# Kernel tuning notes

Measured on AMD Instinct MI355X. Metric: run time of the kernel, lower is better.

The kernel has to match this reference:

```python
import jax, jax.numpy as jnp
import numpy as np

N_NODES = 50000
N_EDGES = 800000
IN_FEAT = 128
HIDDEN = 128
NUM_CLASS = 40


def setup_inputs() -> dict:
    key = jax.random.key(0)
    ks = jax.random.split(key, 8)
    feat = jax.random.normal(ks[0], (N_NODES, IN_FEAT), dtype=jnp.float32)
    # Glorot-ish init scale for reference weights
    W1 = jax.random.normal(ks[1], (IN_FEAT, HIDDEN), dtype=jnp.float32) / np.sqrt(IN_FEAT)
    b1 = jnp.zeros((HIDDEN,), dtype=jnp.float32)
    W2 = jax.random.normal(ks[2], (HIDDEN, HIDDEN), dtype=jnp.float32) / np.sqrt(HIDDEN)
    b2 = jnp.zeros((HIDDEN,), dtype=jnp.float32)
    W3 = jax.random.normal(ks[3], (HIDDEN, NUM_CLASS), dtype=jnp.float32) / np.sqrt(HIDDEN)
    b3 = jnp.zeros((NUM_CLASS,), dtype=jnp.float32)
    src = jax.random.randint(ks[4], (N_EDGES,), 0, N_NODES, dtype=jnp.int32)
    dst = jax.random.randint(ks[5], (N_EDGES,), 0, N_NODES, dtype=jnp.int32)
    return {"feat": feat, "W1": W1, "b1": b1, "W2": W2, "b2": b2,
            "W3": W3, "b3": b3, "src": src, "dst": dst}


def reference(feat, W1, b1, W2, b2, W3, b3, src, dst):
    # symmetric 'both' normalization as in DGL GraphConv:
    # h_dst = deg_in(dst)^{-1/2} * sum_{e:(s->d)} deg_out(s)^{-1/2} * (x_s W) + b
    ones = jnp.ones((src.shape[0],), dtype=feat.dtype)
    out_deg = jax.ops.segment_sum(ones, src, num_segments=N_NODES)
    in_deg = jax.ops.segment_sum(ones, dst, num_segments=N_NODES)
    out_norm = jax.lax.rsqrt(jnp.maximum(out_deg, 1.0))  # [N]
    in_norm = jax.lax.rsqrt(jnp.maximum(in_deg, 1.0))    # [N]

    def gconv(h, W, b):
        h = (h * out_norm[:, None]) @ W                  # [N, d_out]
        agg = jax.ops.segment_sum(h[src], dst, num_segments=N_NODES)
        return agg * in_norm[:, None] + b

    # eval mode: BatchNorm disabled (identity), dropout is a no-op
    h = jax.nn.relu(gconv(feat, W1, b1))
    h = jax.nn.relu(gconv(h, W2, b2))
    return gconv(h, W3, b3)
```

## Files before the change

kernel.cpp:

```cpp
#include <hip/hip_runtime.h>
#include <hip/hip_bf16.h>

#define N_NODES 50000
#define N_EDGES 800000
#define FEAT    128
#define HID     128
#define NCLS    40
#define XPAD    50048

#define RANGE   12500
#define NRANGE  4
#define NS      32
#define SLICE   (N_EDGES / NS)
#define NBLK    49

static constexpr size_t ALIGNB = 256;
static constexpr size_t aln(size_t x){ return (x + ALIGNB - 1) & ~(ALIGNB - 1); }
static constexpr size_t OFF_ONORM   = 0;
static constexpr size_t OFF_INORM   = OFF_ONORM + aln((size_t)N_NODES * 4);
static constexpr size_t OFF_ROWPTR  = OFF_INORM + aln((size_t)N_NODES * 4);
static constexpr size_t OFF_BSUM    = OFF_ROWPTR + aln((size_t)(N_NODES + 1) * 4);
static constexpr size_t OFF_WT1     = OFF_BSUM + aln(64 * 4);
static constexpr size_t OFF_WT2     = OFF_WT1 + aln((size_t)128 * 128 * 2);
static constexpr size_t OFF_WT3     = OFF_WT2 + aln((size_t)128 * 128 * 2);
static constexpr size_t OFF_ESRC    = OFF_WT3 + aln((size_t)64 * 128 * 2);
static constexpr size_t OFF_HTMP    = OFF_ESRC + aln((size_t)N_EDGES * 4);
static constexpr size_t OFF_XBUF    = OFF_HTMP + aln((size_t)XPAD * 128 * 2);
static constexpr size_t OFF_PART    = OFF_HTMP;

__device__ __forceinline__ float bflo(unsigned u){
  union { unsigned i; float f; } c; c.i = u << 16; return c.f;
}
__device__ __forceinline__ float bfhi(unsigned u){
  union { unsigned i; float f; } c; c.i = u & 0xffff0000u; return c.f;
}
__device__ __forceinline__ unsigned pkbf(float a, float b){
  union { __hip_bfloat16 h; unsigned short u; } ca, cb;
  ca.h = __float2bfloat16(a); cb.h = __float2bfloat16(b);
  return ((unsigned)cb.u << 16) | (unsigned)ca.u;
}
__device__ __forceinline__ unsigned short bf1(float a){
  union { __hip_bfloat16 h; unsigned short u; } c;
  c.h = __float2bfloat16(a); return c.u;
}

typedef __attribute__((ext_vector_type(8))) short bf16x8;
typedef __attribute__((ext_vector_type(4))) float f32x4;

__global__ __launch_bounds__(1024) void k_hist_lds(const int* __restrict__ src,
                                                   const int* __restrict__ dst,
                                                   unsigned* __restrict__ part,
                                                   const float* __restrict__ W1,
                                                   const float* __restrict__ W2,
                                                   const float* __restrict__ W3,
                                                   unsigned* __restrict__ wt1,
                                                   unsigned* __restrict__ wt2,
                                                   unsigned* __restrict__ wt3){
  __shared__ unsigned h[RANGE];
  const int s = blockIdx.x, r = blockIdx.y, z = blockIdx.z;
  if (z == 0 && r == 0 && s < 20){
    int idx = s * 1024 + threadIdx.x;
    const float* W; unsigned* Wt; int WC;
    if (idx < 8192)       { W = W1; Wt = wt1; WC = 128; }
    else if (idx < 16384) { W = W2; Wt = wt2; WC = 128; idx -= 8192; }
    else                  { W = W3; Wt = wt3; WC = 40;  idx -= 16384; }
    int c = idx >> 6, kp = idx & 63;
    float v0 = (c < WC) ? W[(size_t)(2 * kp)     * WC + c] : 0.f;
    float v1 = (c < WC) ? W[(size_t)(2 * kp + 1) * WC + c] : 0.f;
    Wt[idx] = pkbf(v0, v1);
  }
  const int* __restrict__ idxp = z ? src : dst;
  const int lo = r * RANGE;
  for (int i = threadIdx.x; i < RANGE; i += 1024) h[i] = 0;
  __syncthreads();
  const int e0 = s * SLICE;
  for (int e = e0 + threadIdx.x; e < e0 + SLICE; e += 1024){
    int v = idxp[e] - lo;
    if ((unsigned)v < RANGE) atomicAdd(&h[v], 1u);
  }
  __syncthreads();
  unsigned* p = part + (((size_t)z * NRANGE + r) * NS + s) * RANGE;
  for (int i = threadIdx.x; i < RANGE; i += 1024) p[i] = h[i];
}

__global__ __launch_bounds__(1024) void k_scan1(const unsigned* __restrict__ part,
                                                int* __restrict__ rowptr,
                                                unsigned* __restrict__ bsum,
                                                float* __restrict__ inorm,
                                                float* __restrict__ onorm){
  __shared__ int wsum[16];
  const int t = threadIdx.x, lane = t & 63, w = t >> 6;
  const int i = blockIdx.x * 1024 + t;
  int v = 0;
  if (i < N_NODES){
    int r = i / RANGE, off = i % RANGE;
    const unsigned* pi = part + ((size_t)r * NS) * RANGE + off;
    const unsigned* po = part + (((size_t)NRANGE + r) * NS) * RANGE + off;
    unsigned si = 0, so = 0;
    #pragma unroll 8
    for (int s = 0; s < NS; ++s){
      si += pi[(size_t)s * RANGE];
      so += po[(size_t)s * RANGE];
    }
    inorm[i] = rsqrtf(fmaxf((float)si, 1.0f));
    onorm[i] = rsqrtf(fmaxf((float)so, 1.0f));
    v = (int)si;
  }
  int x = v;
  #pragma unroll
  for (int off = 1; off < 64; off <<= 1){
    int y = __shfl_up(x, off, 64);
    if (lane >= off) x += y;
  }
  if (lane == 63) wsum[w] = x;
  __syncthreads();
  if (w == 0 && lane < 16){
    int s = wsum[lane];
    #pragma unroll
    for (int off = 1; off < 16; off <<= 1){
      int y = __shfl_up(s, off, 64);
      if (lane >= off) s += y;
    }
    wsum[lane] = s;
  }
  __syncthreads();
  int woff = (w > 0) ? wsum[w - 1] : 0;
  if (i < N_NODES) rowptr[i] = woff + x - v;
  if (t == 0) bsum[blockIdx.x] = (unsigned)wsum[15];
}

__global__ __launch_bounds__(1024) void k_scan3(int* __restrict__ rowptr,
                                                const unsigned* __restrict__ bsum,
                                                unsigned* __restrict__ part){
  __shared__ unsigned sboff, stotal;
  const int t = threadIdx.x;
  if (t < 64){
    int v = (t < NBLK) ? (int)bsum[t] : 0;
    int x = v;
    #pragma unroll
    for (int off = 1; off < 64; off <<= 1){
      int y = __shfl_up(x, off, 64);
      if (t >= off) x += y;
    }
    if (t == (int)blockIdx.x) sboff = (unsigned)(x - v);
    if (t == NBLK - 1) stotal = (unsigned)x;
  }
  __syncthreads();
  const int i = blockIdx.x * 1024 + t;
  if (i < N_NODES){
    int rp = rowptr[i] + (int)sboff;
    rowptr[i] = rp;
    int r = i / RANGE, off = i % RANGE;
    unsigned* p = part + ((size_t)r * NS) * RANGE + off;
    unsigned run = (unsigned)rp;
    #pragma unroll 8
    for (int s = 0; s < NS; ++s){
      unsigned c = p[(size_t)s * RANGE];
      p[(size_t)s * RANGE] = run;
      run += c;
    }
  } else if (i == N_NODES) rowptr[i] = (int)stotal;
}

__global__ __launch_bounds__(1024) void k_scatter_lds(const int* __restrict__ src,
                                                      const int* __restrict__ dst,
                                                      const unsigned* __restrict__ part,
                                                      int* __restrict__ esrc){
  __shared__ unsigned cur[RANGE];
  const int s = blockIdx.x, r = blockIdx.y;
  const int lo = r * RANGE;
  const unsigned* p = part + ((size_t)r * NS + s) * RANGE;
  for (int i = threadIdx.x; i < RANGE; i += 1024) cur[i] = p[i];
  __syncthreads();
  const int e0 = s * SLICE;
  for (int e = e0 + threadIdx.x; e < e0 + SLICE; e += 1024){
    int v = dst[e] - lo;
    if ((unsigned)v < RANGE){
      unsigned pos = atomicAdd(&cur[v], 1u);
      esrc[pos] = src[e];
    }
  }
}

template<int CT, int WCOUT, int OUTC, bool IN_F32>
__global__ __launch_bounds__(256) void k_gemm_mfma(const void* __restrict__ xin,
                                                   const unsigned short* __restrict__ wt,
                                                   const float* __restrict__ onorm,
                                                   unsigned short* __restrict__ outb){
  __shared__ unsigned short Wl[CT * 16][136];
  const int t = threadIdx.x;
  const int lane = t & 63;
  const int w = t >> 6;
  const int ln15 = lane & 15;
  const int quad = lane >> 4;

  {
    const uint4* w4 = (const uint4*)wt;
    #pragma unroll
    for (int i = 0; i < CT; ++i){
      int idx = t + i * 256;
      int row = idx >> 4, q = idx & 15;
      *(uint4*)&Wl[row][q * 8] = w4[idx];
    }
  }
  __syncthreads();

  f32x4 acc[CT];
  #pragma unroll
  for (int ct = 0; ct < CT; ++ct) acc[ct] = (f32x4){0.f, 0.f, 0.f, 0.f};

  const int xr = min(blockIdx.x * 64 + w * 16 + ln15, N_NODES - 1);
  #pragma unroll
  for (int kp = 0; kp < 4; ++kp){
    bf16x8 a;
    if (IN_F32){
      const float4* x4 = (const float4*)xin + (size_t)xr * 32;
      float4 p0 = x4[kp * 8 + quad * 2];
      float4 p1 = x4[kp * 8 + quad * 2 + 1];
      union { bf16x8 v; unsigned u[4]; } ua;
      ua.u[0] = pkbf(p0.x, p0.y); ua.u[1] = pkbf(p0.z, p0.w);
      ua.u[2] = pkbf(p1.x, p1.y); ua.u[3] = pkbf(p1.z, p1.w);
      a = ua.v;
    } else {
      const unsigned short* xrow = (const unsigned short*)xin + (size_t)xr * 128;
      a = *(const bf16x8*)(xrow + kp * 32 + quad * 8);
    }
    #pragma unroll
    for (int ct = 0; ct < CT; ++ct){
      bf16x8 b = *(const bf16x8*)&Wl[ct * 16 + ln15][kp * 32 + quad * 8];
      acc[ct] = __builtin_amdgcn_mfma_f32_16x16x32_bf16(a, b, acc[ct], 0, 0, 0);
    }
  }

  const int rowbase = blockIdx.x * 64 + w * 16 + quad * 4;
  float o[4];
  #pragma unroll
  for (int j = 0; j < 4; ++j){
    int r = rowbase + j;
    o[j] = (r < N_NODES) ? onorm[r] : 0.f;
  }
  #pragma unroll
  for (int ct = 0; ct < CT; ++ct){
    int col = ct * 16 + ln15;
    if (WCOUT < CT * 16 && col >= WCOUT) continue;
    #pragma unroll
    for (int j = 0; j < 4; ++j){
      int r = rowbase + j;
      if (r < N_NODES)
        outb[(size_t)r * OUTC + col] = bf1(acc[ct][j] * o[j]);
    }
  }
}

template<int CW, bool RELU, bool OUTBF>
__global__ __launch_bounds__(256) void k_agg(const unsigned* __restrict__ htmp,
                                             const int* __restrict__ rowptr,
                                             const int* __restrict__ esrc,
                                             const float* __restrict__ inorm,
                                             const float* __restrict__ bias,
                                             void* __restrict__ outv){
  constexpr int CU = CW / 2;
  const int wave = threadIdx.x >> 6;
  const int lane = threadIdx.x & 63;
  const int node = blockIdx.x * 4 + wave;
  if (node >= N_NODES) return;
  const int start = rowptr[node], end = rowptr[node + 1];
  float aL[4] = {0.f, 0.f, 0.f, 0.f};
  float aH[4] = {0.f, 0.f, 0.f, 0.f};
  for (int e0 = start; e0 < end; e0 += 64){
    const int n = min(64, end - e0);
    int el = (lane < n) ? esrc[e0 + lane] : 0;
    int j = 0;
    for (; j + 8 <= n; j += 8){
      int ss[8];
      #pragma unroll
      for (int q = 0; q < 8; ++q) ss[q] = __shfl(el, j + q);
      if (lane < CU){
        unsigned uu[8];
        #pragma unroll
        for (int q = 0; q < 8; ++q) uu[q] = htmp[(size_t)ss[q] * CU + lane];
        #pragma unroll
        for (int q = 0; q < 8; ++q){ aL[q & 3] += bflo(uu[q]); aH[q & 3] += bfhi(uu[q]); }
      }
    }
    for (; j + 4 <= n; j += 4){
      int ss[4];
      #pragma unroll
      for (int q = 0; q < 4; ++q) ss[q] = __shfl(el, j + q);
      if (lane < CU){
        unsigned uu[4];
        #pragma unroll
        for (int q = 0; q < 4; ++q) uu[q] = htmp[(size_t)ss[q] * CU + lane];
        #pragma unroll
        for (int q = 0; q < 4; ++q){ aL[q] += bflo(uu[q]); aH[q] += bfhi(uu[q]); }
      }
    }
    for (; j < n; ++j){
      int s0 = __shfl(el, j);
      if (lane < CU){
        unsigned u0 = htmp[(size_t)s0 * CU + lane];
        aL[0] += bflo(u0); aH[0] += bfhi(u0);
      }
    }
  }
  if (lane < CU){
    float sc = inorm[node];
    float y0 = ((aL[0] + aL[1]) + (aL[2] + aL[3])) * sc + bias[2 * lane];
    float y1 = ((aH[0] + aH[1]) + (aH[2] + aH[3])) * sc + bias[2 * lane + 1];
    if (RELU){ y0 = fmaxf(y0, 0.f); y1 = fmaxf(y1, 0.f); }
    if (OUTBF){
      ((unsigned*)outv)[(size_t)node * CU + lane] = pkbf(y0, y1);
    } else {
      float2 v; v.x = y0; v.y = y1;
      *(float2*)&((float*)outv)[(size_t)node * CW + 2 * lane] = v;
    }
  }
}

extern "C" void kernel_launch(void* const* d_in, const int* in_sizes, int n_in,
                              void* d_out, int out_size, void* d_ws, size_t ws_size,
                              hipStream_t stream){
  const float* feat = (const float*)d_in[0];
  const float* W1   = (const float*)d_in[1];
  const float* b1   = (const float*)d_in[2];
  const float* W2   = (const float*)d_in[3];
  const float* b2   = (const float*)d_in[4];
  const float* W3   = (const float*)d_in[5];
  const float* b3   = (const float*)d_in[6];
  const int* src = (const int*)d_in[7];
  const int* dst = (const int*)d_in[8];
  float* out = (float*)d_out;

  char* ws = (char*)d_ws;
  float*    onorm   = (float*)   (ws + OFF_ONORM);
  float*    inorm   = (float*)   (ws + OFF_INORM);
  int*      rowptr  = (int*)     (ws + OFF_ROWPTR);
  unsigned* bsum    = (unsigned*)(ws + OFF_BSUM);
  unsigned* wt1     = (unsigned*)(ws + OFF_WT1);
  unsigned* wt2     = (unsigned*)(ws + OFF_WT2);
  unsigned* wt3     = (unsigned*)(ws + OFF_WT3);
  int*      esrc    = (int*)     (ws + OFF_ESRC);
  unsigned short* htmp = (unsigned short*)(ws + OFF_HTMP);
  unsigned short* xbuf = (unsigned short*)(ws + OFF_XBUF);
  unsigned* part    = (unsigned*)(ws + OFF_PART);

  k_hist_lds    <<<dim3(NS, NRANGE, 2), 1024, 0, stream>>>(src, dst, part,
                                                           W1, W2, W3, wt1, wt2, wt3);
  k_scan1       <<<NBLK, 1024, 0, stream>>>(part, rowptr, bsum, inorm, onorm);
  k_scan3       <<<NBLK, 1024, 0, stream>>>(rowptr, bsum, part);
  k_scatter_lds <<<dim3(NS, NRANGE), 1024, 0, stream>>>(src, dst, part, esrc);

  const int GB = XPAD / 64;
  const int AB = (N_NODES + 3) / 4;
  k_gemm_mfma<8, 128, 128, true ><<<GB, 256, 0, stream>>>(feat, (unsigned short*)wt1, onorm, htmp);
  k_agg<128, true, true ><<<AB, 256, 0, stream>>>((unsigned*)htmp, rowptr, esrc, inorm, b1, xbuf);
  k_gemm_mfma<8, 128, 128, false><<<GB, 256, 0, stream>>>(xbuf, (unsigned short*)wt2, onorm, htmp);
  k_agg<128, true, true ><<<AB, 256, 0, stream>>>((unsigned*)htmp, rowptr, esrc, inorm, b2, xbuf);
  k_gemm_mfma<4, 40, 40, false><<<GB, 256, 0, stream>>>(xbuf, (unsigned short*)wt3, onorm, htmp);
  k_agg<40, false, false><<<AB, 256, 0, stream>>>((unsigned*)htmp, rowptr, esrc, inorm, b3, out);
}
```

Measured before the change: 243.8 us.

## Fuse CSR build kernels into one cooperative kernel with grid syncs

```diff
diff --git a/kernel.cpp b/kernel.cpp
--- a/kernel.cpp
+++ b/kernel.cpp
@@ -1,5 +1,8 @@
 #include <hip/hip_runtime.h>
 #include <hip/hip_bf16.h>
+#include <hip/hip_cooperative_groups.h>
+
+namespace cg = cooperative_groups;
 
 #define N_NODES 50000
 #define N_EDGES 800000
@@ -47,137 +50,142 @@
 typedef __attribute__((ext_vector_type(8))) short bf16x8;
 typedef __attribute__((ext_vector_type(4))) float f32x4;
 
-__global__ __launch_bounds__(1024) void k_hist_lds(const int* __restrict__ src,
-                                                   const int* __restrict__ dst,
-                                                   unsigned* __restrict__ part,
-                                                   const float* __restrict__ W1,
-                                                   const float* __restrict__ W2,
-                                                   const float* __restrict__ W3,
-                                                   unsigned* __restrict__ wt1,
-                                                   unsigned* __restrict__ wt2,
-                                                   unsigned* __restrict__ wt3){
+__global__ __launch_bounds__(1024) void k_csr(const int* __restrict__ src,
+                                              const int* __restrict__ dst,
+                                              unsigned* __restrict__ part,
+                                              int* __restrict__ rowptr,
+                                              unsigned* __restrict__ bsum,
+                                              float* __restrict__ inorm,
+                                              float* __restrict__ onorm,
+                                              int* __restrict__ esrc,
+                                              const float* __restrict__ W1,
+                                              const float* __restrict__ W2,
+                                              const float* __restrict__ W3,
+                                              unsigned* __restrict__ wt1,
+                                              unsigned* __restrict__ wt2,
+                                              unsigned* __restrict__ wt3){
+  cg::grid_group grid = cg::this_grid();
   __shared__ unsigned h[RANGE];
-  const int s = blockIdx.x, r = blockIdx.y, z = blockIdx.z;
-  if (z == 0 && r == 0 && s < 20){
-    int idx = s * 1024 + threadIdx.x;
-    const float* W; unsigned* Wt; int WC;
-    if (idx < 8192)       { W = W1; Wt = wt1; WC = 128; }
-    else if (idx < 16384) { W = W2; Wt = wt2; WC = 128; idx -= 8192; }
-    else                  { W = W3; Wt = wt3; WC = 40;  idx -= 16384; }
-    int c = idx >> 6, kp = idx & 63;
-    float v0 = (c < WC) ? W[(size_t)(2 * kp)     * WC + c] : 0.f;
-    float v1 = (c < WC) ? W[(size_t)(2 * kp + 1) * WC + c] : 0.f;
-    Wt[idx] = pkbf(v0, v1);
-  }
-  const int* __restrict__ idxp = z ? src : dst;
-  const int lo = r * RANGE;
-  for (int i = threadIdx.x; i < RANGE; i += 1024) h[i] = 0;
-  __syncthreads();
-  const int e0 = s * SLICE;
-  for (int e = e0 + threadIdx.x; e < e0 + SLICE; e += 1024){
-    int v = idxp[e] - lo;
-    if ((unsigned)v < RANGE) atomicAdd(&h[v], 1u);
-  }
-  __syncthreads();
-  unsigned* p = part + (((size_t)z * NRANGE + r) * NS + s) * RANGE;
-  for (int i = threadIdx.x; i < RANGE; i += 1024) p[i] = h[i];
-}
-
-__global__ __launch_bounds__(1024) void k_scan1(const unsigned* __restrict__ part,
-                                                int* __restrict__ rowptr,
-                                                unsigned* __restrict__ bsum,
-                                                float* __restrict__ inorm,
-                                                float* __restrict__ onorm){
   __shared__ int wsum[16];
-  const int t = threadIdx.x, lane = t & 63, w = t >> 6;
-  const int i = blockIdx.x * 1024 + t;
-  int v = 0;
-  if (i < N_NODES){
-    int r = i / RANGE, off = i % RANGE;
-    const unsigned* pi = part + ((size_t)r * NS) * RANGE + off;
-    const unsigned* po = part + (((size_t)NRANGE + r) * NS) * RANGE + off;
-    unsigned si = 0, so = 0;
-    #pragma unroll 8
-    for (int s = 0; s < NS; ++s){
-      si += pi[(size_t)s * RANGE];
-      so += po[(size_t)s * RANGE];
-    }
-    inorm[i] = rsqrtf(fmaxf((float)si, 1.0f));
-    onorm[i] = rsqrtf(fmaxf((float)so, 1.0f));
-    v = (int)si;
-  }
-  int x = v;
-  #pragma unroll
-  for (int off = 1; off < 64; off <<= 1){
-    int y = __shfl_up(x, off, 64);
-    if (lane >= off) x += y;
-  }
-  if (lane == 63) wsum[w] = x;
-  __syncthreads();
-  if (w == 0 && lane < 16){
-    int s = wsum[lane];
-    #pragma unroll
-    for (int off = 1; off < 16; off <<= 1){
-      int y = __shfl_up(s, off, 64);
-      if (lane >= off) s += y;
-    }
-    wsum[lane] = s;
-  }
-  __syncthreads();
-  int woff = (w > 0) ? wsum[w - 1] : 0;
-  if (i < N_NODES) rowptr[i] = woff + x - v;
-  if (t == 0) bsum[blockIdx.x] = (unsigned)wsum[15];
-}
-
-__global__ __launch_bounds__(1024) void k_scan3(int* __restrict__ rowptr,
-                                                const unsigned* __restrict__ bsum,
-                                                unsigned* __restrict__ part){
   __shared__ unsigned sboff, stotal;
   const int t = threadIdx.x;
-  if (t < 64){
-    int v = (t < NBLK) ? (int)bsum[t] : 0;
+  const int b = blockIdx.x;
+
+  {
+    const int s = b & 31;
+    const int r = (b >> 5) & 3;
+    const int z = b >> 7;
+    if (z == 0 && r == 0 && s < 20){
+      int idx = s * 1024 + t;
+      const float* W; unsigned* Wt; int WC;
+      if (idx < 8192)       { W = W1; Wt = wt1; WC = 128; }
+      else if (idx < 16384) { W = W2; Wt = wt2; WC = 128; idx -= 8192; }
+      else                  { W = W3; Wt = wt3; WC = 40;  idx -= 16384; }
+      int c = idx >> 6, kp = idx & 63;
+      float v0 = (c < WC) ? W[(size_t)(2 * kp)     * WC + c] : 0.f;
+      float v1 = (c < WC) ? W[(size_t)(2 * kp + 1) * WC + c] : 0.f;
+      Wt[idx] = pkbf(v0, v1);
+    }
+    const int* __restrict__ idxp = z ? src : dst;
+    const int lo = r * RANGE;
+    for (int i = t; i < RANGE; i += 1024) h[i] = 0;
+    __syncthreads();
+    const int e0 = s * SLICE;
+    for (int e = e0 + t; e < e0 + SLICE; e += 1024){
+      int v = idxp[e] - lo;
+      if ((unsigned)v < RANGE) atomicAdd(&h[v], 1u);
+    }
+    __syncthreads();
+    unsigned* p = part + (((size_t)z * NRANGE + r) * NS + s) * RANGE;
+    for (int i = t; i < RANGE; i += 1024) p[i] = h[i];
+  }
+  grid.sync();
+
+  if (b < NBLK){
+    const int lane = t & 63, w = t >> 6;
+    const int i = b * 1024 + t;
+    int v = 0;
+    if (i < N_NODES){
+      int r = i / RANGE, off = i % RANGE;
+      const unsigned* pi = part + ((size_t)r * NS) * RANGE + off;
+      const unsigned* po = part + (((size_t)NRANGE + r) * NS) * RANGE + off;
+      unsigned si = 0, so = 0;
+      #pragma unroll 8
+      for (int s = 0; s < NS; ++s){
+        si += pi[(size_t)s * RANGE];
+        so += po[(size_t)s * RANGE];
+      }
+      inorm[i] = rsqrtf(fmaxf((float)si, 1.0f));
+      onorm[i] = rsqrtf(fmaxf((float)so, 1.0f));
+      v = (int)si;
+    }
     int x = v;
     #pragma unroll
     for (int off = 1; off < 64; off <<= 1){
       int y = __shfl_up(x, off, 64);
-      if (t >= off) x += y;
-    }
-    if (t == (int)blockIdx.x) sboff = (unsigned)(x - v);
-    if (t == NBLK - 1) stotal = (unsigned)x;
-  }
-  __syncthreads();
-  const int i = blockIdx.x * 1024 + t;
-  if (i < N_NODES){
-    int rp = rowptr[i] + (int)sboff;
-    rowptr[i] = rp;
-    int r = i / RANGE, off = i % RANGE;
-    unsigned* p = part + ((size_t)r * NS) * RANGE + off;
-    unsigned run = (unsigned)rp;
-    #pragma unroll 8
-    for (int s = 0; s < NS; ++s){
-      unsigned c = p[(size_t)s * RANGE];
-      p[(size_t)s * RANGE] = run;
-      run += c;
-    }
-  } else if (i == N_NODES) rowptr[i] = (int)stotal;
-}
-
-__global__ __launch_bounds__(1024) void k_scatter_lds(const int* __restrict__ src,
-                                                      const int* __restrict__ dst,
-                                                      const unsigned* __restrict__ part,
-                                                      int* __restrict__ esrc){
-  __shared__ unsigned cur[RANGE];
-  const int s = blockIdx.x, r = blockIdx.y;
-  const int lo = r * RANGE;
-  const unsigned* p = part + ((size_t)r * NS + s) * RANGE;
-  for (int i = threadIdx.x; i < RANGE; i += 1024) cur[i] = p[i];
-  __syncthreads();
-  const int e0 = s * SLICE;
-  for (int e = e0 + threadIdx.x; e < e0 + SLICE; e += 1024){
-    int v = dst[e] - lo;
-    if ((unsigned)v < RANGE){
-      unsigned pos = atomicAdd(&cur[v], 1u);
-      esrc[pos] = src[e];
+      if (lane >= off) x += y;
+    }
+    if (lane == 63) wsum[w] = x;
+    __syncthreads();
+    if (w == 0 && lane < 16){
+      int s = wsum[lane];
+      #pragma unroll
+      for (int off = 1; off < 16; off <<= 1){
+        int y = __shfl_up(s, off, 64);
+        if (lane >= off) s += y;
+      }
+      wsum[lane] = s;
+    }
+    __syncthreads();
+    int woff = (w > 0) ? wsum[w - 1] : 0;
+    if (i < N_NODES) rowptr[i] = woff + x - v;
+    if (t == 0) bsum[b] = (unsigned)wsum[15];
+  }
+  grid.sync();
+
+  if (b < NBLK){
+    if (t < 64){
+      int v = (t < NBLK) ? (int)bsum[t] : 0;
+      int x = v;
+      #pragma unroll
+      for (int off = 1; off < 64; off <<= 1){
+        int y = __shfl_up(x, off, 64);
+        if (t >= off) x += y;
+      }
+      if (t == b) sboff = (unsigned)(x - v);
+      if (t == NBLK - 1) stotal = (unsigned)x;
+    }
+    __syncthreads();
+    const int i = b * 1024 + t;
+    if (i < N_NODES){
+      int rp = rowptr[i] + (int)sboff;
+      rowptr[i] = rp;
+      int r = i / RANGE, off = i % RANGE;
+      unsigned* p = part + ((size_t)r * NS) * RANGE + off;
+      unsigned run = (unsigned)rp;
+      #pragma unroll 8
+      for (int s = 0; s < NS; ++s){
+        unsigned c = p[(size_t)s * RANGE];
+        p[(size_t)s * RANGE] = run;
+        run += c;
+      }
+    } else if (i == N_NODES) rowptr[i] = (int)stotal;
+  }
+  grid.sync();
+
+  if (b < NS * NRANGE){
+    const int s = b & 31, r = b >> 5;
+    const int lo = r * RANGE;
+    const unsigned* p = part + ((size_t)r * NS + s) * RANGE;
+    for (int i = t; i < RANGE; i += 1024) h[i] = p[i];
+    __syncthreads();
+    const int e0 = s * SLICE;
+    for (int e = e0 + t; e < e0 + SLICE; e += 1024){
+      int v = dst[e] - lo;
+      if ((unsigned)v < RANGE){
+        unsigned pos = atomicAdd(&h[v], 1u);
+        esrc[pos] = src[e];
+      }
     }
   }
 }
@@ -344,11 +352,12 @@
   unsigned short* xbuf = (unsigned short*)(ws + OFF_XBUF);
   unsigned* part    = (unsigned*)(ws + OFF_PART);
 
-  k_hist_lds    <<<dim3(NS, NRANGE, 2), 1024, 0, stream>>>(src, dst, part,
-                                                           W1, W2, W3, wt1, wt2, wt3);
-  k_scan1       <<<NBLK, 1024, 0, stream>>>(part, rowptr, bsum, inorm, onorm);
-  k_scan3       <<<NBLK, 1024, 0, stream>>>(rowptr, bsum, part);
-  k_scatter_lds <<<dim3(NS, NRANGE), 1024, 0, stream>>>(src, dst, part, esrc);
+  void* kargs[] = {(void*)&src, (void*)&dst, (void*)&part, (void*)&rowptr, (void*)&bsum,
+                   (void*)&inorm, (void*)&onorm, (void*)&esrc,
+                   (void*)&W1, (void*)&W2, (void*)&W3,
+                   (void*)&wt1, (void*)&wt2, (void*)&wt3};
+  hipLaunchCooperativeKernel((void*)k_csr, dim3(NS * NRANGE * 2), dim3(1024),
+                             kargs, 0, stream);
 
   const int GB = XPAD / 64;
   const int AB = (N_NODES + 3) / 4;
```

After: 358.7 us. +47.1%, slower.
